# Performance work log

Hardware: AMD Instinct MI355X
Metric: run time of the kernel (lower is better)

Reference implementation:

```python
import jax, jax.numpy as jnp
import numpy as np

VOCAB = 8192
DIM = 64
COMMITMENT = 0.25
N = 65536


def setup_inputs() -> dict:
    key = jax.random.key(0)
    kx, ke = jax.random.split(key)
    x = jax.random.normal(kx, (N, DIM), dtype=jnp.float32)
    # matches nn.Embedding weight init uniform_(-0.5, 0.5)
    emb_weight = jax.random.uniform(ke, (VOCAB, DIM), dtype=jnp.float32, minval=-0.5, maxval=0.5)
    return {"x": x, "emb_weight": emb_weight}


def reference(x, emb_weight):
    # cdist(x, E, p=2): squared form gives identical argmin (sqrt is monotone)
    x2 = jnp.sum(x * x, axis=-1, keepdims=True)            # [N, 1]
    e2 = jnp.sum(emb_weight * emb_weight, axis=-1)         # [V]
    d2 = x2 + e2[None, :] - 2.0 * (x @ emb_weight.T)       # [N, V]
    idx = jnp.argmin(d2, axis=-1)                          # [N] int

    quantised = emb_weight[idx]                            # [N, D] gather

    codebook_loss = jnp.mean((quantised - jax.lax.stop_gradient(x)) ** 2)
    e_latent_loss = jnp.mean((jax.lax.stop_gradient(quantised) - x) ** 2)
    loss = codebook_loss + COMMITMENT * e_latent_loss

    # straight-through estimator
    quantised_ste = x + jax.lax.stop_gradient(quantised - x)
    return quantised_ste, loss, idx
```

## Files before the change

kernel.cpp:

```cpp
#include <hip/hip_runtime.h>

#define N 65536
#define D 64
#define V 8192
#define LOSS_OFF (N * D)
#define IDX_OFF (N * D + 1)
#define MARGIN 0.02f
#define NPART 4

typedef _Float16 half8 __attribute__((ext_vector_type(8)));
typedef float f32x4 __attribute__((ext_vector_type(4)));

typedef __attribute__((address_space(1))) const void gas_t;
typedef __attribute__((address_space(3))) void las_t;

#define DOT16(s, A0, A1, A2, A3, B0, B1, B2, B3)                         \
    s = fmaf(A0.x, B0.x, s); s = fmaf(A0.y, B0.y, s);                    \
    s = fmaf(A0.z, B0.z, s); s = fmaf(A0.w, B0.w, s);                    \
    s = fmaf(A1.x, B1.x, s); s = fmaf(A1.y, B1.y, s);                    \
    s = fmaf(A1.z, B1.z, s); s = fmaf(A1.w, B1.w, s);                    \
    s = fmaf(A2.x, B2.x, s); s = fmaf(A2.y, B2.y, s);                    \
    s = fmaf(A2.z, B2.z, s); s = fmaf(A2.w, B2.w, s);                    \
    s = fmaf(A3.x, B3.x, s); s = fmaf(A3.y, B3.y, s);                    \
    s = fmaf(A3.z, B3.z, s); s = fmaf(A3.w, B3.w, s);

__device__ __forceinline__ unsigned enc32(float f) {
    unsigned u = __float_as_uint(f);
    return (u & 0x80000000u) ? ~u : (u | 0x80000000u);
}

__global__ __launch_bounds__(256) void k_split(const float* __restrict__ E,
                                               _Float16* __restrict__ Ef16,
                                               float* __restrict__ e2,
                                               float* __restrict__ dout,
                                               int* __restrict__ fcount) {
    const int t = blockIdx.x * 256 + threadIdx.x;
    if (t == 0) {
        dout[LOSS_OFF] = 0.0f;
        *fcount = 0;
    }
    const int row = t >> 3;
    const int seg = t & 7;
    const float4* p = (const float4*)(E + (size_t)row * D + seg * 8);
    float4 a = p[0], b = p[1];
    float s = a.x * a.x + a.y * a.y + a.z * a.z + a.w * a.w +
              b.x * b.x + b.y * b.y + b.z * b.z + b.w * b.w;
    s += __shfl_xor(s, 1, 8);
    s += __shfl_xor(s, 2, 8);
    s += __shfl_xor(s, 4, 8);
    if (seg == 0) e2[row] = s;
    half8 h;
    h[0] = (_Float16)(-2.0f * a.x); h[1] = (_Float16)(-2.0f * a.y);
    h[2] = (_Float16)(-2.0f * a.z); h[3] = (_Float16)(-2.0f * a.w);
    h[4] = (_Float16)(-2.0f * b.x); h[5] = (_Float16)(-2.0f * b.y);
    h[6] = (_Float16)(-2.0f * b.z); h[7] = (_Float16)(-2.0f * b.w);
    *(half8*)(Ef16 + (size_t)row * D + seg * 8) = h;
}

#define MERGE(M1, M2, GID, L, PID)          \
    {                                       \
        bool bt = (L) < (M1);               \
        float m2c = bt ? (M1) : (L);        \
        (M2) = fminf((M2), m2c);            \
        (GID) = bt ? (PID) : (GID);         \
        (M1) = fminf((M1), (L));            \
    }

__global__ __launch_bounds__(512) void k_argmin(const float* __restrict__ X,
                                                const _Float16* __restrict__ Ef16,
                                                const float* __restrict__ e2,
                                                float4* __restrict__ part4) {
    __shared__ __align__(16) _Float16 els[2][8192];

    const int tid = threadIdx.x;
    const int lane = tid & 63;
    const int wave = tid >> 6;
    const int P = blockIdx.x & 3;
    const int rb = blockIdx.x >> 2;
    const int c4 = lane & 15;
    const int kg = lane >> 4;
    const int wrow = rb * 256 + wave * 32;
    const int sw = c4 & 7;
    const int k0off = (kg ^ sw) * 8;
    const int k1off = ((4 + kg) ^ sw) * 8;
    const int ch0 = P * 16;

    half8 x00, x01, x10, x11;
    {
        const float* xr0 = X + (size_t)(wrow + c4) * D;
        const float* xr1 = X + (size_t)(wrow + 16 + c4) * D;
#pragma unroll
        for (int f = 0; f < 2; ++f) {
            float4 lo = *(const float4*)(xr0 + f * 32 + kg * 8);
            float4 hi = *(const float4*)(xr0 + f * 32 + kg * 8 + 4);
            half8 h;
            h[0] = (_Float16)lo.x; h[1] = (_Float16)lo.y;
            h[2] = (_Float16)lo.z; h[3] = (_Float16)lo.w;
            h[4] = (_Float16)hi.x; h[5] = (_Float16)hi.y;
            h[6] = (_Float16)hi.z; h[7] = (_Float16)hi.w;
            if (f == 0) x00 = h; else x01 = h;
        }
#pragma unroll
        for (int f = 0; f < 2; ++f) {
            float4 lo = *(const float4*)(xr1 + f * 32 + kg * 8);
            float4 hi = *(const float4*)(xr1 + f * 32 + kg * 8 + 4);
            half8 h;
            h[0] = (_Float16)lo.x; h[1] = (_Float16)lo.y;
            h[2] = (_Float16)lo.z; h[3] = (_Float16)lo.w;
            h[4] = (_Float16)hi.x; h[5] = (_Float16)hi.y;
            h[6] = (_Float16)hi.z; h[7] = (_Float16)hi.w;
            if (f == 0) x10 = h; else x11 = h;
        }
    }

    const int q0 = tid, q1 = tid + 512;
    const _Float16* gs0 = Ef16 + (size_t)(ch0 * 128 + (q0 >> 3)) * 64 + ((q0 & 7) ^ ((q0 >> 3) & 7)) * 8;
    const _Float16* gs1 = Ef16 + (size_t)(ch0 * 128 + (q1 >> 3)) * 64 + ((q1 & 7) ^ ((q1 >> 3) & 7)) * 8;
    const int ld0 = q0 * 8, ld1 = q1 * 8;

#define STAGE(BUF)                                                            \
    {                                                                         \
        __builtin_amdgcn_global_load_lds((gas_t*)gs0, (las_t*)&els[BUF][ld0], 16, 0, 0); \
        __builtin_amdgcn_global_load_lds((gas_t*)gs1, (las_t*)&els[BUF][ld1], 16, 0, 0); \
        gs0 += 8192; gs1 += 8192;                                             \
    }

    float m1a = 3.4e38f, m2a = 3.4e38f, m1b = 3.4e38f, m2b = 3.4e38f;
    unsigned gida = 0, gidb = 0;

#define TSTEP(T, E2Q)                                                         \
    {                                                                         \
        const half8 a0 = *(const half8*)&els[buf][(T * 16 + c4) * 64 + k0off];\
        const half8 a1 = *(const half8*)&els[buf][(T * 16 + c4) * 64 + k1off];\
        f32x4 acc0 = __builtin_amdgcn_mfma_f32_16x16x32_f16(a0, x00, E2Q, 0, 0, 0); \
        acc0 = __builtin_amdgcn_mfma_f32_16x16x32_f16(a1, x01, acc0, 0, 0, 0);\
        f32x4 acc1 = __builtin_amdgcn_mfma_f32_16x16x32_f16(a0, x10, E2Q, 0, 0, 0); \
        acc1 = __builtin_amdgcn_mfma_f32_16x16x32_f16(a1, x11, acc1, 0, 0, 0);\
        La = fminf(fminf(fminf(fminf(La, acc0[0]), acc0[1]), acc0[2]), acc0[3]); \
        Lb = fminf(fminf(fminf(fminf(Lb, acc1[0]), acc1[1]), acc1[2]), acc1[3]); \
    }

    STAGE(0)
    const f32x4* e2p = (const f32x4*)(e2 + (size_t)ch0 * 128) + kg;
    unsigned pidb = (unsigned)(ch0 * 8 + kg);

    for (int ci = 0; ci < 16; ++ci) {
        __syncthreads();
        const f32x4 e2q0 = e2p[0],  e2q1 = e2p[4],  e2q2 = e2p[8],  e2q3 = e2p[12];
        const f32x4 e2q4 = e2p[16], e2q5 = e2p[20], e2q6 = e2p[24], e2q7 = e2p[28];
        e2p += 32;
        if (ci < 15) STAGE((ci + 1) & 1)
        const int buf = ci & 1;

        float La = 3.4e38f, Lb = 3.4e38f;
        TSTEP(0, e2q0) TSTEP(1, e2q1) TSTEP(2, e2q2) TSTEP(3, e2q3)
        MERGE(m1a, m2a, gida, La, pidb)
        MERGE(m1b, m2b, gidb, Lb, pidb)
        La = 3.4e38f; Lb = 3.4e38f;
        TSTEP(4, e2q4) TSTEP(5, e2q5) TSTEP(6, e2q6) TSTEP(7, e2q7)
        MERGE(m1a, m2a, gida, La, pidb + 4)
        MERGE(m1b, m2b, gidb, Lb, pidb + 4)
        pidb += 8;
    }

#pragma unroll
    for (int off = 16; off < 64; off <<= 1) {
        float o1, o2;
        unsigned og;
        o1 = __shfl_xor(m1a, off, 64); o2 = __shfl_xor(m2a, off, 64);
        og = (unsigned)__shfl_xor((int)gida, off, 64);
        m2a = fminf(fminf(fmaxf(m1a, o1), m2a), o2);
        if (o1 < m1a) gida = og;
        m1a = fminf(m1a, o1);
        o1 = __shfl_xor(m1b, off, 64); o2 = __shfl_xor(m2b, off, 64);
        og = (unsigned)__shfl_xor((int)gidb, off, 64);
        m2b = fminf(fminf(fmaxf(m1b, o1), m2b), o2);
        if (o1 < m1b) gidb = og;
        m1b = fminf(m1b, o1);
    }

    if (lane < 16) {
        float4 r;
        r.x = m1a; r.y = m2a; r.z = __uint_as_float(gida); r.w = 0.0f;
        part4[(size_t)P * N + wrow + lane] = r;
        r.x = m1b; r.y = m2b; r.z = __uint_as_float(gidb);
        part4[(size_t)P * N + wrow + 16 + lane] = r;
    }
}

__global__ __launch_bounds__(256) void k_group(const float* __restrict__ X,
                                               const float* __restrict__ E,
                                               const float* __restrict__ e2,
                                               const float4* __restrict__ part4,
                                               int* __restrict__ fcount,
                                               int* __restrict__ flist,
                                               unsigned long long* __restrict__ packed,
                                               float* __restrict__ lpart,
                                               float* __restrict__ dout) {
    const int lane = threadIdx.x & 63;
    const int wave = threadIdx.x >> 6;
    const int lig = lane & 15;
    const int grp = lane >> 4;
    const int row = blockIdx.x * 16 + wave * 4 + grp;

    float m1, m2;
    unsigned g;
    {
        const float4 r0 = part4[row];
        m1 = r0.x; m2 = r0.y; g = __float_as_uint(r0.z);
#pragma unroll
        for (int k = 1; k < NPART; ++k) {
            const float4 r = part4[(size_t)k * N + row];
            const unsigned rg = __float_as_uint(r.z);
            if (r.x < m1) {
                m2 = fminf(m2, m1);
                m1 = r.x;
                g = rg;
            } else {
                m2 = fminf(m2, r.x);
            }
            m2 = fminf(m2, r.y);
        }
    }

    float lossp = 0.0f;
    if (m2 - m1 < MARGIN) {
        if (lig == 0) {
            int p = atomicAdd(fcount, 1);
            flist[p] = row;
            packed[p] = ~0ull;
        }
    } else {
        const int es = lig >> 2;
        const int dg = lig & 3;
        const int base = (int)((g >> 3) * 128 + ((g >> 2) & 1) * 64 +
                               (g & 3) * 4 + es);
        const float4* xp = (const float4*)(X + (size_t)row * D) + dg * 4;
        float4 xa0 = xp[0], xa1 = xp[1], xa2 = xp[2], xa3 = xp[3];

        float best = 3.4e38f;
        int bidx = 0x7fffffff;
#pragma unroll
        for (int eg = 0; eg < 4; ++eg) {
            const int v = base + eg * 16;
            const float4* ep = (const float4*)(E + (size_t)v * D) + dg * 4;
            float4 b0 = ep[0], b1 = ep[1], b2 = ep[2], b3 = ep[3];
            float s = 0.0f;
            DOT16(s, xa0, xa1, xa2, xa3, b0, b1, b2, b3)
            s += __shfl_xor(s, 1, 64);
            s += __shfl_xor(s, 2, 64);
            float d = fmaf(-2.0f, s, e2[v]);
            if (d < best) { best = d; bidx = v; }
        }
#pragma unroll
        for (int off = 4; off < 16; off <<= 1) {
            float ob = __shfl_xor(best, off, 64);
            int oi = __shfl_xor(bidx, off, 64);
            if (ob < best || (ob == best && oi < bidx)) { best = ob; bidx = oi; }
        }
        if (lig == 0) dout[IDX_OFF + row] = (float)bidx;
        float4 x4 = *(const float4*)(X + (size_t)row * D + lig * 4);
        float4 q4 = *(const float4*)(E + (size_t)bidx * D + lig * 4);
        float4 o;
        o.x = x4.x + (q4.x - x4.x);
        o.y = x4.y + (q4.y - x4.y);
        o.z = x4.z + (q4.z - x4.z);
        o.w = x4.w + (q4.w - x4.w);
        *(float4*)(dout + (size_t)row * D + lig * 4) = o;
        float dx = q4.x - x4.x, dy = q4.y - x4.y, dz = q4.z - x4.z,
              dw = q4.w - x4.w;
        lossp = dx * dx + dy * dy + dz * dz + dw * dw;
    }

#pragma unroll
    for (int off = 32; off; off >>= 1) lossp += __shfl_down(lossp, off, 64);
    __shared__ float ps[4];
    if (lane == 0) ps[wave] = lossp;
    __syncthreads();
    if (threadIdx.x == 0) lpart[blockIdx.x] = ps[0] + ps[1] + ps[2] + ps[3];
}

__global__ __launch_bounds__(256) void k_full(const float* __restrict__ X,
                                              const float* __restrict__ E,
                                              const float* __restrict__ e2,
                                              const int* __restrict__ fcount,
                                              const int* __restrict__ flist,
                                              unsigned long long* __restrict__ packed) {
    const int nf = *fcount;
    if (nf == 0) return;
    const int nq = (nf + 3) >> 2;
    const int total = nq * 8;
    const int lane = threadIdx.x & 63;
    const int nwaves = gridDim.x * 4;
    int item = blockIdx.x * 4 + (threadIdx.x >> 6);
    const int e4 = lane >> 2;
    const int dg = lane & 3;

    for (; item < total; item += nwaves) {
        const int qi = item >> 3;
        const int c = item & 7;
        const int f0 = qi * 4;
        const int f1 = min(f0 + 1, nf - 1);
        const int f2 = min(f0 + 2, nf - 1);
        const int f3 = min(f0 + 3, nf - 1);
        const int r0 = flist[f0], r1 = flist[f1], r2 = flist[f2], r3 = flist[f3];

        const float4* xp0 = (const float4*)(X + (size_t)r0 * D) + dg * 4;
        const float4* xp1 = (const float4*)(X + (size_t)r1 * D) + dg * 4;
        const float4* xp2 = (const float4*)(X + (size_t)r2 * D) + dg * 4;
        const float4* xp3 = (const float4*)(X + (size_t)r3 * D) + dg * 4;
        float4 xa0 = xp0[0], xa1 = xp0[1], xa2 = xp0[2], xa3 = xp0[3];
        float4 xb0 = xp1[0], xb1 = xp1[1], xb2 = xp1[2], xb3 = xp1[3];
        float4 xc0 = xp2[0], xc1 = xp2[1], xc2 = xp2[2], xc3 = xp2[3];
        float4 xd0 = xp3[0], xd1 = xp3[1], xd2 = xp3[2], xd3 = xp3[3];

        unsigned long long k0 = ~0ull, k1 = ~0ull, k2 = ~0ull, k3 = ~0ull;

#pragma unroll 2
        for (int it = 0; it < 64; ++it) {
            const int v = c * 1024 + it * 16 + e4;
            const float4* ep = (const float4*)(E + (size_t)v * D) + dg * 4;
            float4 b0 = ep[0], b1 = ep[1], b2 = ep[2], b3 = ep[3];
            float s0 = 0.0f, s1 = 0.0f, s2 = 0.0f, s3 = 0.0f;
            DOT16(s0, xa0, xa1, xa2, xa3, b0, b1, b2, b3)
            DOT16(s1, xb0, xb1, xb2, xb3, b0, b1, b2, b3)
            DOT16(s2, xc0, xc1, xc2, xc3, b0, b1, b2, b3)
            DOT16(s3, xd0, xd1, xd2, xd3, b0, b1, b2, b3)
            s0 += __shfl_xor(s0, 1, 64); s0 += __shfl_xor(s0, 2, 64);
            s1 += __shfl_xor(s1, 1, 64); s1 += __shfl_xor(s1, 2, 64);
            s2 += __shfl_xor(s2, 1, 64); s2 += __shfl_xor(s2, 2, 64);
            s3 += __shfl_xor(s3, 1, 64); s3 += __shfl_xor(s3, 2, 64);
            const float ev = e2[v];
            const unsigned long long vb = (unsigned long long)(unsigned)v;
            unsigned long long t;
            t = ((unsigned long long)enc32(fmaf(-2.0f, s0, ev)) << 32) | vb;
            k0 = t < k0 ? t : k0;
            t = ((unsigned long long)enc32(fmaf(-2.0f, s1, ev)) << 32) | vb;
            k1 = t < k1 ? t : k1;
            t = ((unsigned long long)enc32(fmaf(-2.0f, s2, ev)) << 32) | vb;
            k2 = t < k2 ? t : k2;
            t = ((unsigned long long)enc32(fmaf(-2.0f, s3, ev)) << 32) | vb;
            k3 = t < k3 ? t : k3;
        }

#pragma unroll
        for (int off = 4; off < 64; off <<= 1) {
            unsigned lo, hi;
            unsigned long long o;
            lo = __shfl_xor((unsigned)k0, off, 64); hi = __shfl_xor((unsigned)(k0 >> 32), off, 64);
            o = ((unsigned long long)hi << 32) | lo; k0 = o < k0 ? o : k0;
            lo = __shfl_xor((unsigned)k1, off, 64); hi = __shfl_xor((unsigned)(k1 >> 32), off, 64);
            o = ((unsigned long long)hi << 32) | lo; k1 = o < k1 ? o : k1;
            lo = __shfl_xor((unsigned)k2, off, 64); hi = __shfl_xor((unsigned)(k2 >> 32), off, 64);
            o = ((unsigned long long)hi << 32) | lo; k2 = o < k2 ? o : k2;
            lo = __shfl_xor((unsigned)k3, off, 64); hi = __shfl_xor((unsigned)(k3 >> 32), off, 64);
            o = ((unsigned long long)hi << 32) | lo; k3 = o < k3 ? o : k3;
        }

        if (lane == 0) {
            atomicMin(&packed[f0], k0);
            atomicMin(&packed[f1], k1);
            atomicMin(&packed[f2], k2);
            atomicMin(&packed[f3], k3);
        }
    }
}

__global__ __launch_bounds__(256) void k_out2(const float* __restrict__ X,
                                              const float* __restrict__ E,
                                              const int* __restrict__ fcount,
                                              const int* __restrict__ flist,
                                              const unsigned long long* __restrict__ packed,
                                              const float* __restrict__ lpart,
                                              float* __restrict__ dout) {
    const int lane = threadIdx.x & 63;
    const int wave = threadIdx.x >> 6;
    float lossp = 0.0f;
    if (wave == 0) lossp += lpart[blockIdx.x * 64 + lane];

    const int nf = *fcount;
    const int nwaves = gridDim.x * 4;
    for (int i = blockIdx.x * 4 + wave; i < nf; i += nwaves) {
        const int row = flist[i];
        const int idx = (int)(unsigned)(packed[i] & 0xffffffffull);
        if (lane == 0) dout[IDX_OFF + row] = (float)idx;
        if (lane < 16) {
            float4 x4 = *(const float4*)(X + (size_t)row * D + lane * 4);
            float4 q4 = *(const float4*)(E + (size_t)idx * D + lane * 4);
            float4 o;
            o.x = x4.x + (q4.x - x4.x);
            o.y = x4.y + (q4.y - x4.y);
            o.z = x4.z + (q4.z - x4.z);
            o.w = x4.w + (q4.w - x4.w);
            *(float4*)(dout + (size_t)row * D + lane * 4) = o;
            float dx = q4.x - x4.x, dy = q4.y - x4.y, dz = q4.z - x4.z,
                  dw = q4.w - x4.w;
            lossp += dx * dx + dy * dy + dz * dz + dw * dw;
        }
    }

#pragma unroll
    for (int off = 32; off; off >>= 1) lossp += __shfl_down(lossp, off, 64);
    __shared__ float ps[4];
    if (lane == 0) ps[wave] = lossp;
    __syncthreads();
    if (threadIdx.x == 0) {
        float tot = ps[0] + ps[1] + ps[2] + ps[3];
        atomicAdd(dout + LOSS_OFF, tot * (1.25f / ((float)N * (float)D)));
    }
}

extern "C" void kernel_launch(void* const* d_in, const int* in_sizes, int n_in,
                              void* d_out, int out_size, void* d_ws,
                              size_t ws_size, hipStream_t stream) {
    const float* X = (const float*)d_in[0];
    const float* E = (const float*)d_in[1];
    float* out = (float*)d_out;

    char* ws = (char*)d_ws;
    _Float16* Ef16 = (_Float16*)ws;
    float* e2 = (float*)(ws + 1048576);
    int* fcount = (int*)(ws + 1081344);
    int* flist = (int*)(ws + 1081600);
    unsigned long long* packed = (unsigned long long*)(ws + 1343744);
    float* lpart = (float*)(ws + 1868032);
    float4* part4 = (float4*)(ws + 1933568);

    k_split<<<256, 256, 0, stream>>>(E, Ef16, e2, out, fcount);
    k_argmin<<<(N / 256) * NPART, 512, 0, stream>>>(X, Ef16, e2, part4);
    k_group<<<N / 16, 256, 0, stream>>>(X, E, e2, part4, fcount, flist, packed, lpart, out);
    k_full<<<1024, 256, 0, stream>>>(X, E, e2, fcount, flist, packed);
    k_out2<<<64, 256, 0, stream>>>(X, E, fcount, flist, packed, lpart, out);
}
```

Measured before the change: 182.1 us.

## Shrink argmin blocks to 256 threads and stage e2 through LDS

```diff
diff --git a/kernel.cpp b/kernel.cpp
--- a/kernel.cpp
+++ b/kernel.cpp
@@ -66,11 +66,12 @@
         (M1) = fminf((M1), (L));            \
     }
 
-__global__ __launch_bounds__(512) void k_argmin(const float* __restrict__ X,
+__global__ __launch_bounds__(256) void k_argmin(const float* __restrict__ X,
                                                 const _Float16* __restrict__ Ef16,
                                                 const float* __restrict__ e2,
                                                 float4* __restrict__ part4) {
-    __shared__ __align__(16) _Float16 els[2][8192];
+    __shared__ __align__(16) _Float16 els[2][4096];
+    __shared__ __align__(16) float e2ls[2][64];
 
     const int tid = threadIdx.x;
     const int lane = tid & 63;
@@ -79,11 +80,11 @@
     const int rb = blockIdx.x >> 2;
     const int c4 = lane & 15;
     const int kg = lane >> 4;
-    const int wrow = rb * 256 + wave * 32;
+    const int wrow = rb * 128 + wave * 32;
     const int sw = c4 & 7;
     const int k0off = (kg ^ sw) * 8;
     const int k1off = ((4 + kg) ^ sw) * 8;
-    const int ch0 = P * 16;
+    const int vbase = P * 2048;
 
     half8 x00, x01, x10, x11;
     {
@@ -113,54 +114,52 @@
         }
     }
 
-    const int q0 = tid, q1 = tid + 512;
-    const _Float16* gs0 = Ef16 + (size_t)(ch0 * 128 + (q0 >> 3)) * 64 + ((q0 & 7) ^ ((q0 >> 3) & 7)) * 8;
-    const _Float16* gs1 = Ef16 + (size_t)(ch0 * 128 + (q1 >> 3)) * 64 + ((q1 & 7) ^ ((q1 >> 3) & 7)) * 8;
-    const int ld0 = q0 * 8, ld1 = q1 * 8;
+    const int q0 = tid, q1 = tid + 256;
+    const _Float16* gs0 = Ef16 + (size_t)(vbase + (q0 >> 3)) * 64 + ((q0 & 7) ^ ((q0 >> 3) & 7)) * 8;
+    const _Float16* gs1 = Ef16 + (size_t)(vbase + (q1 >> 3)) * 64 + ((q1 & 7) ^ ((q1 >> 3) & 7)) * 8;
+    const float* ge2 = e2 + vbase + (tid & 15) * 4;
+    const int ld0 = q0 * 8, ld1 = q1 * 8, lde = (tid & 15) * 4;
+    const bool do_e2 = (tid < 16);
 
 #define STAGE(BUF)                                                            \
     {                                                                         \
         __builtin_amdgcn_global_load_lds((gas_t*)gs0, (las_t*)&els[BUF][ld0], 16, 0, 0); \
         __builtin_amdgcn_global_load_lds((gas_t*)gs1, (las_t*)&els[BUF][ld1], 16, 0, 0); \
-        gs0 += 8192; gs1 += 8192;                                             \
+        if (do_e2)                                                            \
+            __builtin_amdgcn_global_load_lds((gas_t*)ge2,                     \
+                                             (las_t*)&e2ls[BUF][lde], 16, 0, 0); \
+        gs0 += 4096; gs1 += 4096; ge2 += 64;                                  \
     }
 
     float m1a = 3.4e38f, m2a = 3.4e38f, m1b = 3.4e38f, m2b = 3.4e38f;
     unsigned gida = 0, gidb = 0;
 
-#define TSTEP(T, E2Q)                                                         \
+#define TSTEP(T)                                                              \
     {                                                                         \
+        const f32x4 e2q = *(const f32x4*)&e2ls[buf][T * 16 + kg * 4];         \
         const half8 a0 = *(const half8*)&els[buf][(T * 16 + c4) * 64 + k0off];\
         const half8 a1 = *(const half8*)&els[buf][(T * 16 + c4) * 64 + k1off];\
-        f32x4 acc0 = __builtin_amdgcn_mfma_f32_16x16x32_f16(a0, x00, E2Q, 0, 0, 0); \
+        f32x4 acc0 = __builtin_amdgcn_mfma_f32_16x16x32_f16(a0, x00, e2q, 0, 0, 0); \
         acc0 = __builtin_amdgcn_mfma_f32_16x16x32_f16(a1, x01, acc0, 0, 0, 0);\
-        f32x4 acc1 = __builtin_amdgcn_mfma_f32_16x16x32_f16(a0, x10, E2Q, 0, 0, 0); \
+        f32x4 acc1 = __builtin_amdgcn_mfma_f32_16x16x32_f16(a0, x10, e2q, 0, 0, 0); \
         acc1 = __builtin_amdgcn_mfma_f32_16x16x32_f16(a1, x11, acc1, 0, 0, 0);\
         La = fminf(fminf(fminf(fminf(La, acc0[0]), acc0[1]), acc0[2]), acc0[3]); \
         Lb = fminf(fminf(fminf(fminf(Lb, acc1[0]), acc1[1]), acc1[2]), acc1[3]); \
     }
 
     STAGE(0)
-    const f32x4* e2p = (const f32x4*)(e2 + (size_t)ch0 * 128) + kg;
-    unsigned pidb = (unsigned)(ch0 * 8 + kg);
-
-    for (int ci = 0; ci < 16; ++ci) {
+    unsigned pidb = (unsigned)(P * 128 + kg);
+
+    for (int ci = 0; ci < 32; ++ci) {
         __syncthreads();
-        const f32x4 e2q0 = e2p[0],  e2q1 = e2p[4],  e2q2 = e2p[8],  e2q3 = e2p[12];
-        const f32x4 e2q4 = e2p[16], e2q5 = e2p[20], e2q6 = e2p[24], e2q7 = e2p[28];
-        e2p += 32;
-        if (ci < 15) STAGE((ci + 1) & 1)
+        if (ci < 31) STAGE((ci + 1) & 1)
         const int buf = ci & 1;
 
         float La = 3.4e38f, Lb = 3.4e38f;
-        TSTEP(0, e2q0) TSTEP(1, e2q1) TSTEP(2, e2q2) TSTEP(3, e2q3)
+        TSTEP(0) TSTEP(1) TSTEP(2) TSTEP(3)
         MERGE(m1a, m2a, gida, La, pidb)
         MERGE(m1b, m2b, gidb, Lb, pidb)
-        La = 3.4e38f; Lb = 3.4e38f;
-        TSTEP(4, e2q4) TSTEP(5, e2q5) TSTEP(6, e2q6) TSTEP(7, e2q7)
-        MERGE(m1a, m2a, gida, La, pidb + 4)
-        MERGE(m1b, m2b, gidb, Lb, pidb + 4)
-        pidb += 8;
+        pidb += 4;
     }
 
 #pragma unroll
@@ -233,8 +232,7 @@
     } else {
         const int es = lig >> 2;
         const int dg = lig & 3;
-        const int base = (int)((g >> 3) * 128 + ((g >> 2) & 1) * 64 +
-                               (g & 3) * 4 + es);
+        const int base = (int)((g >> 2) * 64 + (g & 3) * 4 + es);
         const float4* xp = (const float4*)(X + (size_t)row * D) + dg * 4;
         float4 xa0 = xp[0], xa1 = xp[1], xa2 = xp[2], xa3 = xp[3];
 
@@ -427,7 +425,7 @@
     float4* part4 = (float4*)(ws + 1933568);
 
     k_split<<<256, 256, 0, stream>>>(E, Ef16, e2, out, fcount);
-    k_argmin<<<(N / 256) * NPART, 512, 0, stream>>>(X, Ef16, e2, part4);
+    k_argmin<<<(N / 128) * NPART, 256, 0, stream>>>(X, Ef16, e2, part4);
     k_group<<<N / 16, 256, 0, stream>>>(X, E, e2, part4, fcount, flist, packed, lpart, out);
     k_full<<<1024, 256, 0, stream>>>(X, E, e2, fcount, flist, packed);
     k_out2<<<64, 256, 0, stream>>>(X, E, fcount, flist, packed, lpart, out);
```

After: 187.2 us. 2.8% more time.
